# Optimization experiments

Measured on AMD Instinct MI355X. Metric: run time of the kernel, lower is better.

Reference implementation:

```python
import jax, jax.numpy as jnp
import numpy as np

N_NODES = 100000
N_EDGES = 1600000
HIDDEN = 64
N_LAYERS = 3
N_CLASSES = 2
N_GRAPHS = 128
NEG_SLOPE = 0.2  # PyG GATConv default negative_slope


def setup_inputs() -> dict:
    key = jax.random.key(0)
    ks = jax.random.split(key, 8)
    x = jax.random.randint(ks[0], (N_NODES,), 0, 2)
    edge_index = jax.random.randint(ks[1], (2, N_EDGES), 0, N_NODES)
    batch = jnp.sort(jax.random.randint(ks[2], (N_NODES,), 0, N_GRAPHS))
    scale = 1.0 / np.sqrt(HIDDEN)
    embed_table = jax.random.normal(ks[3], (2, HIDDEN), jnp.float32)
    Ws = jax.random.normal(ks[4], (N_LAYERS, HIDDEN, HIDDEN), jnp.float32) * scale
    a_srcs = jax.random.normal(ks[5], (N_LAYERS, HIDDEN), jnp.float32) * scale
    a_dsts = jax.random.normal(ks[6], (N_LAYERS, HIDDEN), jnp.float32) * scale
    biases = jnp.zeros((N_LAYERS, HIDDEN), jnp.float32)
    W_out = jax.random.normal(ks[7], (HIDDEN, N_CLASSES), jnp.float32) * scale
    b_out = jnp.zeros((N_CLASSES,), jnp.float32)
    return {"x": x, "edge_index": edge_index, "batch": batch,
            "embed_table": embed_table, "Ws": Ws, "a_srcs": a_srcs,
            "a_dsts": a_dsts, "biases": biases, "W_out": W_out, "b_out": b_out}


def _gat_layer(h, src, dst, W, a_s, a_d, b):
    # h: [N, D]; src/dst: [E'] (self loops included) -> PyG GATConv, heads=1
    hW = h @ W                                   # [N, D]
    e = jax.nn.leaky_relu((hW @ a_s)[src] + (hW @ a_d)[dst], NEG_SLOPE)  # [E']
    m = jax.ops.segment_max(e, dst, num_segments=N_NODES)               # stable softmax per dst
    ex = jnp.exp(e - m[dst])
    denom = jax.ops.segment_sum(ex, dst, num_segments=N_NODES)
    alpha = ex / denom[dst]                      # [E']
    out = jax.ops.segment_sum(hW[src] * alpha[:, None], dst, num_segments=N_NODES)
    return out + b


def reference(x, edge_index, batch, embed_table, Ws, a_srcs, a_dsts, biases, W_out, b_out):
    loop = jnp.arange(N_NODES)
    src = jnp.concatenate([edge_index[0], loop])  # PyG add_self_loops=True
    dst = jnp.concatenate([edge_index[1], loop])
    h = embed_table[x]                            # [N, D]
    for l in range(N_LAYERS):
        h = _gat_layer(h, src, dst, Ws[l], a_srcs[l], a_dsts[l], biases[l])
        if l < N_LAYERS - 1:
            h = jax.nn.relu(h)
    sums = jax.ops.segment_sum(h, batch, num_segments=N_GRAPHS)
    counts = jax.ops.segment_sum(jnp.ones((N_NODES,), h.dtype), batch, num_segments=N_GRAPHS)
    pooled = sums / jnp.maximum(counts, 1.0)[:, None]  # global_mean_pool
    return pooled @ W_out + b_out                      # [G, num_classes]
```

## Files before the change

### kernel.cpp

```cpp
#include <hip/hip_runtime.h>
#include <hip/hip_bf16.h>
#include <float.h>

#define N_NODES 100000
#define N_EDGES 1600000
#define HIDDEN 64
#define N_GRAPHS 128
#define NEG_SLOPE 0.2f
#define ETOT (N_EDGES + N_NODES)

#define BSHIFT 9
#define NB ((N_NODES + 511) >> BSHIFT)
#define PAIR_CHUNK 4096
#define PAIR_BLOCKS ((N_EDGES + PAIR_CHUNK - 1) / PAIR_CHUNK)
#define XBIT_BLOCKS ((N_NODES + 255) / 256)
#define TBL_BLOCKS (NLVL / 8)
#define CAP 12288

#define NREP 64
#define REP_STRIDE 272
#define NLVL 512

__device__ __forceinline__ unsigned short f2bf(float f) {
    unsigned u = __float_as_uint(f);
    unsigned r = (u + 0x7FFFu + ((u >> 16) & 1u)) >> 16;
    return (unsigned short)r;
}
__device__ __forceinline__ float blo(unsigned u) { return __uint_as_float(u << 16); }
__device__ __forceinline__ float bhi(unsigned u) { return __uint_as_float(u & 0xFFFF0000u); }
__device__ __forceinline__ int sb0(unsigned u) { return (int)((unsigned)(u << 24)) >> 24; }
__device__ __forceinline__ int sb1(unsigned u) { return (int)((unsigned)(u << 16)) >> 24; }
__device__ __forceinline__ int sb2(unsigned u) { return (int)((unsigned)(u << 8)) >> 24; }
__device__ __forceinline__ int sb3(unsigned u) { return (int)u >> 24; }


__global__ __launch_bounds__(256) void k_prep(
    const int* __restrict__ x,
    int* __restrict__ gcnt, float* __restrict__ pool_acc,
    unsigned* __restrict__ xb)
{
    int t = threadIdx.x, b = blockIdx.x;
    if (b == 0 && t < NB) gcnt[t] = 0;
    if (b < NREP && t < 2 * N_GRAPHS) pool_acc[b * REP_STRIDE + t] = 0.f;
    int i = b * 256 + t;
    int lane = t & 63;
    bool bb = (i < N_NODES) && (x[i] != 0);
    unsigned long long m = __ballot(bb);
    int wid = i >> 6;
    if (i < N_NODES + 64) {
        if (lane == 0) xb[wid * 2] = (unsigned)m;
        if (lane == 32) xb[wid * 2 + 1] = (unsigned)(m >> 32);
    }
}


__global__ __launch_bounds__(512) void k_scatter(
    const int* __restrict__ e0, const int* __restrict__ e1,
    const unsigned* __restrict__ xb, int* __restrict__ gcnt,
    int* __restrict__ pairs,
    const float* __restrict__ embed, const float* __restrict__ Ws,
    const float* __restrict__ biases, const float* __restrict__ a_srcs,
    const float* __restrict__ a_dsts, const float* __restrict__ W_out,
    unsigned char* __restrict__ Tq8, float* __restrict__ Tscl,
    float* __restrict__ Ts1s, float* __restrict__ Ts1d,
    float* __restrict__ sparams)
{
    __shared__ int hcnt[NB];
    __shared__ int base[NB];
    __shared__ int lstart[NB];
    __shared__ int tot[256];
    __shared__ int staged[PAIR_CHUNK];
    __shared__ int sdest[PAIR_CHUNK];
    int t = threadIdx.x, b = blockIdx.x;

    if (b >= PAIR_BLOCKS) {
        int l = (b - PAIR_BLOCKS) * 8 + (t >> 6);
        int f = t & 63;
        float r0 = 0.f, r1 = 0.f;
#pragma unroll 8
        for (int k = 0; k < 64; ++k) {
            float w = Ws[k * 64 + f];
            r0 = fmaf(embed[k], w, r0);
            r1 = fmaf(embed[64 + k], w, r1);
        }
        if (l == 0) {
            float as = a_srcs[f], ad = a_dsts[f];
            float t0 = r0 * as, t1 = r1 * as, t2 = r0 * ad, t3 = r1 * ad;
#pragma unroll
            for (int off = 32; off >= 1; off >>= 1) {
                t0 += __shfl_xor(t0, off); t1 += __shfl_xor(t1, off);
                t2 += __shfl_xor(t2, off); t3 += __shfl_xor(t3, off);
            }
            if (f == 0) { sparams[0] = t0; sparams[1] = t1; sparams[2] = t2; sparams[3] = t3; }
        }
        if (l == 1) {
            float b2 = biases[128 + f];
            float t4 = b2 * W_out[f * 2];
            float t5 = b2 * W_out[f * 2 + 1];
#pragma unroll
            for (int off = 32; off >= 1; off >>= 1) {
                t4 += __shfl_xor(t4, off); t5 += __shfl_xor(t5, off);
            }
            if (f == 0) { sparams[4] = t4; sparams[5] = t5; }
        }
        float c1 = (float)l * (1.f / (NLVL - 1));
        float o = fmaxf(biases[f] + r0 + c1 * (r1 - r0), 0.f);
        const float* W1 = Ws + 4096;
        float h = 0.f;
#pragma unroll 8
        for (int k = 0; k < 64; ++k) h = fmaf(__shfl(o, k), W1[k * 64 + f], h);
        float ss = h * a_srcs[64 + f];
        float sd = h * a_dsts[64 + f];
        float am = fabsf(h);
#pragma unroll
        for (int off = 32; off >= 1; off >>= 1) {
            ss += __shfl_xor(ss, off);
            sd += __shfl_xor(sd, off);
            am = fmaxf(am, __shfl_xor(am, off));
        }
        float iscl = (am > 0.f) ? 127.f / am : 0.f;
        Tq8[l * 64 + f] = (unsigned char)(__float2int_rn(h * iscl) & 255);
        if (f == 0) { Tscl[l] = am * (1.f / 127.f); Ts1s[l] = ss; Ts1d[l] = sd; }
        return;
    }

    if (t < NB) hcnt[t] = 0;
    __syncthreads();
    int ebase = b * PAIR_CHUNK;
    int ecount = min(PAIR_CHUNK, N_EDGES - ebase);
    for (int i = 4 * t; i < ecount; i += 2048) {
        int4 d4 = *(const int4*)(e1 + ebase + i);
        atomicAdd(&hcnt[d4.x >> BSHIFT], 1);
        atomicAdd(&hcnt[d4.y >> BSHIFT], 1);
        atomicAdd(&hcnt[d4.z >> BSHIFT], 1);
        atomicAdd(&hcnt[d4.w >> BSHIFT], 1);
    }
    __syncthreads();
    int v = (t < NB) ? hcnt[t] : 0;
    if (t < 256) tot[t] = v;
    __syncthreads();
    for (int off = 1; off < 256; off <<= 1) {
        int u = (t >= off && t < 256) ? tot[t - off] : 0;
        __syncthreads();
        if (t < 256) tot[t] += u;
        __syncthreads();
    }
    if (t < NB) {
        lstart[t] = tot[t] - v;
        base[t] = v ? atomicAdd(&gcnt[t], v) : 0;
        hcnt[t] = 0;
    }
    __syncthreads();
    for (int i = 4 * t; i < ecount; i += 2048) {
        int4 s4 = *(const int4*)(e0 + ebase + i);
        int4 d4 = *(const int4*)(e1 + ebase + i);
        int ss[4] = {s4.x, s4.y, s4.z, s4.w};
        int dd[4] = {d4.x, d4.y, d4.z, d4.w};
#pragma unroll
        for (int j = 0; j < 4; ++j) {
            int s = ss[j], d = dd[j];
            int xv = (xb[s >> 5] >> (s & 31)) & 1;
            int B = d >> BSHIFT;
            int idx = atomicAdd(&hcnt[B], 1);
            int lp = lstart[B] + idx;
            staged[lp] = (xv << 26) | ((d & 511) << 17) | s;
            sdest[lp] = B * CAP + base[B] + idx;
        }
    }
    __syncthreads();
    for (int i = t; i < ecount; i += 512)
        pairs[sdest[i]] = staged[i];
}

__global__ __launch_bounds__(1024) void k_csr_bucket(
    const int* __restrict__ pairs, const int* __restrict__ gcnt,
    const int* __restrict__ x, const float* __restrict__ sparams,
    int* __restrict__ rowptr, int* __restrict__ col,
    unsigned short* __restrict__ cidx)
{
    __shared__ int deg[512];
    __shared__ int excl[512];
    __shared__ int cnt2[512];
    __shared__ int wsum[16];
    __shared__ int p0sh;
    int b = blockIdx.x;
    int t = threadIdx.x;
    int nb = b << BSHIFT;
    int nodes = min(512, N_NODES - nb);

    int pv = (t < b) ? gcnt[t] : 0;
#pragma unroll
    for (int off = 32; off >= 1; off >>= 1) pv += __shfl_xor(pv, off);
    if ((t & 63) == 0) wsum[t >> 6] = pv;
    __syncthreads();
    if (t == 0) {
        int s = 0;
#pragma unroll
        for (int i = 0; i < 16; ++i) s += wsum[i];
        p0sh = s;
    }

    int xself = 0;
    if (t < 512) {
        xself = (t < nodes) ? (x[nb + t] & 1) : 0;
        deg[t] = (t < nodes) ? (1 | (xself << 16)) : 0;
        cnt2[t] = 1;
    }
    __syncthreads();
    int cnt = gcnt[b];
    int pbase = b * CAP;
    int cnt4 = cnt & ~3;
    for (int i = 4 * t; i < cnt4; i += 4096) {
        int4 p4 = *(const int4*)(pairs + pbase + i);
        atomicAdd(&deg[(p4.x >> 17) & 511], 1 | (((p4.x >> 26) & 1) << 16));
        atomicAdd(&deg[(p4.y >> 17) & 511], 1 | (((p4.y >> 26) & 1) << 16));
        atomicAdd(&deg[(p4.z >> 17) & 511], 1 | (((p4.z >> 26) & 1) << 16));
        atomicAdd(&deg[(p4.w >> 17) & 511], 1 | (((p4.w >> 26) & 1) << 16));
    }
    for (int i = cnt4 + t; i < cnt; i += 1024) {
        int p = pairs[pbase + i];
        atomicAdd(&deg[(p >> 17) & 511], 1 | (((p >> 26) & 1) << 16));
    }
    __syncthreads();

    int packed = (t < 512) ? deg[t] : 0;
    int val = packed & 0xFFFF;
    int kx = packed >> 16;
    if (t < nodes) {
        float ss0 = sparams[0], ss1 = sparams[1];
        float sd = xself ? sparams[3] : sparams[2];
        float e0 = ss0 + sd; e0 = (e0 >= 0.f) ? e0 : NEG_SLOPE * e0;
        float e1 = ss1 + sd; e1 = (e1 >= 0.f) ? e1 : NEG_SLOPE * e1;
        float pp0 = __expf(e0), pp1 = __expf(e1);
        float kn = (float)kx, dn = (float)(val - kx);
        float c1 = kn * pp1 / (dn * pp0 + kn * pp1);
        cidx[nb + t] = (unsigned short)__float2int_rn(c1 * (float)(NLVL - 1));
    }

    int xx = val;
#pragma unroll
    for (int off = 1; off < 64; off <<= 1) {
        int y = __shfl_up(xx, off);
        if ((t & 63) >= off) xx += y;
    }
    if ((t & 63) == 63 && t < 512) wsum[t >> 6] = xx;
    __syncthreads();
    if (t == 0) {
        int s = 0;
#pragma unroll
        for (int i = 0; i < 8; ++i) { int v = wsum[i]; wsum[i] = s; s += v; }
    }
    __syncthreads();
    int ex = xx - val + wsum[t >> 6];
    if (t < 512) excl[t] = ex;

    int p0 = p0sh;
    int colbase = p0 + nb;
    if (t < nodes) {
        rowptr[nb + t] = colbase + ex;
        col[colbase + ex] = nb + t;
    }
    if (b == NB - 1 && t == 0) rowptr[N_NODES] = ETOT;
    __syncthreads();
    for (int i = 4 * t; i < cnt4; i += 4096) {
        int4 p4 = *(const int4*)(pairs + pbase + i);
        int pp[4] = {p4.x, p4.y, p4.z, p4.w};
#pragma unroll
        for (int j = 0; j < 4; ++j) {
            int li = (pp[j] >> 17) & 511;
            int pos = colbase + excl[li] + atomicAdd(&cnt2[li], 1);
            col[pos] = pp[j] & 0x1FFFF;
        }
    }
    for (int i = cnt4 + t; i < cnt; i += 1024) {
        int p = pairs[pbase + i];
        int li = (p >> 17) & 511;
        int pos = colbase + excl[li] + atomicAdd(&cnt2[li], 1);
        col[pos] = p & 0x1FFFF;
    }
}


__global__ __launch_bounds__(256) void k_agg1(
    const unsigned char* __restrict__ Tq8, const float* __restrict__ Tscl,
    const float* __restrict__ Ts1s, const float* __restrict__ Ts1d,
    const unsigned short* __restrict__ cidx, const int* __restrict__ col,
    const int* __restrict__ rowptr, const float* __restrict__ bias,
    unsigned short* __restrict__ hout)
{
    __shared__ float2 stash[4][64];
    int t = threadIdx.x;
    int wave = t >> 6, lane = t & 63;
    int h = lane >> 5, hl = lane & 31;
    int base = blockIdx.x * 8 + wave * 2;
    if (base >= N_NODES) return;
    const char* hb = (const char*)Tq8;

    int node = base + h;
    bool valid = (node < N_NODES);
    int row = 0, end = 0;
    if (valid) { row = rowptr[node]; end = rowptr[node + 1]; }
    int deg = end - row;
    int degO = __shfl_xor(deg, 32);
    bool fast = (deg <= 32) && (degO <= 32);

    if (fast) {
        int idx = 0;
        float p = 0.f, sc = 0.f;
        if (hl < deg) idx = cidx[col[row + hl]];
        float sdi = Ts1d[__shfl(idx, h * 32)];
        if (hl < deg) {
            float ee = Ts1s[idx] + sdi;
            ee = (ee >= 0.f) ? ee : NEG_SLOPE * ee;
            p = __expf(ee);
            sc = Tscl[idx];
        }
        stash[wave][lane] = make_float2(p * sc, __int_as_float(idx * 64));

        int q = hl >> 4;
        int f = hl & 15;
        int f4 = f * 4;
        int sb = h * 32;
        float a0 = 0.f, a1 = 0.f, a2 = 0.f, a3 = 0.f;
        int degr = (deg + 7) & ~7;
        for (int j = q; j < degr; j += 8) {
            float2 e0 = stash[wave][sb + j];
            float2 e1 = stash[wave][sb + j + 2];
            float2 e2 = stash[wave][sb + j + 4];
            float2 e3 = stash[wave][sb + j + 6];
            unsigned v0 = *(const unsigned*)(hb + (__float_as_int(e0.y) + f4));
            unsigned v1 = *(const unsigned*)(hb + (__float_as_int(e1.y) + f4));
            unsigned v2 = *(const unsigned*)(hb + (__float_as_int(e2.y) + f4));
            unsigned v3 = *(const unsigned*)(hb + (__float_as_int(e3.y) + f4));
            a0 = fmaf(e0.x, (float)sb0(v0), a0);
            a1 = fmaf(e0.x, (float)sb1(v0), a1);
            a2 = fmaf(e0.x, (float)sb2(v0), a2);
            a3 = fmaf(e0.x, (float)sb3(v0), a3);
            a0 = fmaf(e1.x, (float)sb0(v1), a0);
            a1 = fmaf(e1.x, (float)sb1(v1), a1);
            a2 = fmaf(e1.x, (float)sb2(v1), a2);
            a3 = fmaf(e1.x, (float)sb3(v1), a3);
            a0 = fmaf(e2.x, (float)sb0(v2), a0);
            a1 = fmaf(e2.x, (float)sb1(v2), a1);
            a2 = fmaf(e2.x, (float)sb2(v2), a2);
            a3 = fmaf(e2.x, (float)sb3(v2), a3);
            a0 = fmaf(e3.x, (float)sb0(v3), a0);
            a1 = fmaf(e3.x, (float)sb1(v3), a1);
            a2 = fmaf(e3.x, (float)sb2(v3), a2);
            a3 = fmaf(e3.x, (float)sb3(v3), a3);
        }
        float denom = p;
#pragma unroll
        for (int off = 16; off >= 1; off >>= 1) denom += __shfl_xor(denom, off);
        float inv = 1.f / denom;
        a0 += __shfl_xor(a0, 16);
        a1 += __shfl_xor(a1, 16);
        a2 += __shfl_xor(a2, 16);
        a3 += __shfl_xor(a3, 16);
        if (hl < 16 && valid) {
            float4 bb = *(const float4*)&bias[4 * f];
            ushort4 pk;
            pk.x = f2bf(fmaxf(fmaf(a0, inv, bb.x), 0.f));
            pk.y = f2bf(fmaxf(fmaf(a1, inv, bb.y), 0.f));
            pk.z = f2bf(fmaxf(fmaf(a2, inv, bb.z), 0.f));
            pk.w = f2bf(fmaxf(fmaf(a3, inv, bb.w), 0.f));
            *(ushort4*)&hout[node * 64 + 4 * f] = pk;
        }
    } else {
        for (int s = 0; s < 2; ++s) {
            int nd = base + s;
            if (nd >= N_NODES) continue;
            int r = rowptr[nd], e = rowptr[nd + 1];
            float sdi = Ts1d[cidx[nd]];
            float m = -FLT_MAX;
            for (int j = r + lane; j < e; j += 64) {
                float ee = Ts1s[cidx[col[j]]] + sdi;
                ee = (ee >= 0.f) ? ee : NEG_SLOPE * ee;
                m = fmaxf(m, ee);
            }
#pragma unroll
            for (int off = 32; off >= 1; off >>= 1) m = fmaxf(m, __shfl_xor(m, off));
            float denom = 0.f;
            for (int j = r + lane; j < e; j += 64) {
                float ee = Ts1s[cidx[col[j]]] + sdi;
                ee = (ee >= 0.f) ? ee : NEG_SLOPE * ee;
                denom += __expf(ee - m);
            }
#pragma unroll
            for (int off = 32; off >= 1; off >>= 1) denom += __shfl_xor(denom, off);
            float inv = 1.f / denom;
            float acc = 0.f;
            for (int j = r; j < e; ++j) {
                int idxj = cidx[col[j]];
                float ee = Ts1s[idxj] + sdi;
                ee = (ee >= 0.f) ? ee : NEG_SLOPE * ee;
                float w = __expf(ee - m) * inv * Tscl[idxj];
                int bq = (int)(signed char)Tq8[idxj * 64 + lane];
                acc = fmaf(w, (float)bq, acc);
            }
            hout[nd * 64 + lane] = f2bf(fmaxf(acc + bias[lane], 0.f));
        }
    }
}


__global__ __launch_bounds__(256) void k_gemm2(
    const unsigned* __restrict__ h32, const float* __restrict__ W,
    const float* __restrict__ a_s, const float* __restrict__ a_d,
    const float* __restrict__ W_out,
    float4* __restrict__ szz)
{
    __shared__ float Wl[64 * 64];
    __shared__ float hT[64 * 68];
    int t = threadIdx.x;
    int r0 = blockIdx.x * 64;

    for (int i = t; i < 4096; i += 256) Wl[i] = W[i];
    for (int i = t; i < 2048; i += 256) {
        int r = i >> 5, m = i & 31;
        int row = r0 + r;
        unsigned u = (row < N_NODES) ? h32[row * 32 + m] : 0u;
        hT[(2 * m) * 68 + r]     = blo(u);
        hT[(2 * m + 1) * 68 + r] = bhi(u);
    }
    __syncthreads();

    int tcol = t & 15;
    int trow = t >> 4;
    float acc[4][4];
#pragma unroll
    for (int i = 0; i < 4; ++i)
#pragma unroll
        for (int j = 0; j < 4; ++j) acc[i][j] = 0.f;

    for (int k = 0; k < 64; ++k) {
        float4 va = *(const float4*)&hT[k * 68 + trow * 4];
        float4 vb = *(const float4*)&Wl[k * 64 + tcol * 4];
        float a[4] = {va.x, va.y, va.z, va.w};
        float bb[4] = {vb.x, vb.y, vb.z, vb.w};
#pragma unroll
        for (int i = 0; i < 4; ++i)
#pragma unroll
            for (int j = 0; j < 4; ++j) acc[i][j] = fmaf(a[i], bb[j], acc[i][j]);
    }

    float4 as4 = *(const float4*)&a_s[tcol * 4];
    float4 ad4 = *(const float4*)&a_d[tcol * 4];
    float asr[4] = {as4.x, as4.y, as4.z, as4.w};
    float adr[4] = {ad4.x, ad4.y, ad4.z, ad4.w};
    float4 wa = *(const float4*)&W_out[8 * tcol];
    float4 wb = *(const float4*)&W_out[8 * tcol + 4];

#pragma unroll
    for (int i = 0; i < 4; ++i) {
        int row = r0 + trow * 4 + i;
        float ps = 0.f, pd = 0.f;
#pragma unroll
        for (int j = 0; j < 4; ++j) {
            ps = fmaf(acc[i][j], asr[j], ps);
            pd = fmaf(acc[i][j], adr[j], pd);
        }
        float z0 = acc[i][0] * wa.x + acc[i][1] * wa.z + acc[i][2] * wb.x + acc[i][3] * wb.z;
        float z1 = acc[i][0] * wa.y + acc[i][1] * wa.w + acc[i][2] * wb.y + acc[i][3] * wb.w;
#pragma unroll
        for (int off = 8; off >= 1; off >>= 1) {
            ps += __shfl_xor(ps, off);
            pd += __shfl_xor(pd, off);
            z0 += __shfl_xor(z0, off);
            z1 += __shfl_xor(z1, off);
        }
        if (row < N_NODES && tcol == 0) {
            szz[row] = make_float4(ps, z0, z1, pd);
        }
    }
}


__global__ __launch_bounds__(256) void k_pool2(
    const float4* __restrict__ szz, const int* __restrict__ col,
    const int* __restrict__ rowptr, const int* __restrict__ batch,
    float* __restrict__ pool_acc)
{
    __shared__ int rp2[33];
    int t = threadIdx.x;
    int wave = t >> 6, lane = t & 63;
    int h = lane >> 5, hl = lane & 31;
    int nb0 = blockIdx.x * 32;
    if (t < 33) {
        int n = nb0 + t;
        rp2[t] = (n <= N_NODES) ? rowptr[n] : ETOT;
    }
    __syncthreads();
    float* rep = pool_acc + ((blockIdx.x * 4 + wave) & (NREP - 1)) * REP_STRIDE;

    int gcur = -1;
    float acc0 = 0.f, acc1 = 0.f;

#pragma unroll
    for (int i = 0; i < 4; ++i) {
        int nls = wave * 8 + 2 * i + h;
        int node = nb0 + nls;
        bool valid = (node < N_NODES);
        int row = valid ? rp2[nls] : 0;
        int end = valid ? rp2[nls + 1] : 0;
        int deg = end - row;
        int degO = __shfl_xor(deg, 32);
        bool fast = (deg <= 32) && (degO <= 32);
        float r0 = 0.f, r1 = 0.f;

        if (fast) {
            float sdi = valid ? szz[node].w : 0.f;
            float p = 0.f, zy = 0.f, zz = 0.f;
            if (hl < deg) {
                int c = col[row + hl];
                float4 sz = szz[c];
                float ee = sz.x + sdi;
                ee = (ee >= 0.f) ? ee : NEG_SLOPE * ee;
                p = __expf(ee);
                zy = sz.y; zz = sz.z;
            }
            float n0 = p * zy, n1 = p * zz, dn = p;
#pragma unroll
            for (int off = 16; off >= 1; off >>= 1) {
                n0 += __shfl_xor(n0, off);
                n1 += __shfl_xor(n1, off);
                dn += __shfl_xor(dn, off);
            }
            float inv = 1.f / dn;
            r0 = n0 * inv; r1 = n1 * inv;
        } else {
            float rr0[2], rr1[2];
#pragma unroll
            for (int s = 0; s < 2; ++s) {
                rr0[s] = rr1[s] = 0.f;
                int nds = wave * 8 + 2 * i + s;
                int nd = nb0 + nds;
                if (nd >= N_NODES) continue;
                int r = rp2[nds], e = rp2[nds + 1];
                float sdi = szz[nd].w;
                float n0 = 0.f, n1 = 0.f, dn = 0.f;
                for (int j = r + lane; j < e; j += 64) {
                    int c = col[j];
                    float4 sz = szz[c];
                    float ee = sz.x + sdi;
                    ee = (ee >= 0.f) ? ee : NEG_SLOPE * ee;
                    float p = __expf(ee);
                    n0 = fmaf(p, sz.y, n0);
                    n1 = fmaf(p, sz.z, n1);
                    dn += p;
                }
#pragma unroll
                for (int off = 32; off >= 1; off >>= 1) {
                    n0 += __shfl_xor(n0, off);
                    n1 += __shfl_xor(n1, off);
                    dn += __shfl_xor(dn, off);
                }
                float inv = 1.f / dn;
                rr0[s] = n0 * inv; rr1[s] = n1 * inv;
            }
            r0 = rr0[h]; r1 = rr1[h];
        }

        if (hl == 0 && valid) {
            int g = batch[node];
            if (g != gcur) {
                if (gcur >= 0) {
                    atomicAdd(&rep[gcur * 2], acc0);
                    atomicAdd(&rep[gcur * 2 + 1], acc1);
                }
                gcur = g; acc0 = r0; acc1 = r1;
            } else {
                acc0 += r0; acc1 += r1;
            }
        }
    }
    if (hl == 0 && gcur >= 0) {
        atomicAdd(&rep[gcur * 2], acc0);
        atomicAdd(&rep[gcur * 2 + 1], acc1);
    }
}


__device__ __forceinline__ int lower_bound_dev(const int* __restrict__ a, int n, int v) {
    int lo = 0, hi = n;
    while (lo < hi) {
        int mid = (lo + hi) >> 1;
        if (a[mid] < v) lo = mid + 1; else hi = mid;
    }
    return lo;
}

__global__ void k_head(const float* __restrict__ pool_acc,
                       const int* __restrict__ batch,
                       const float* __restrict__ b_out,
                       const float* __restrict__ sparams,
                       float* __restrict__ out)
{
    int t = threadIdx.x;
    if (t < 2 * N_GRAPHS) {
        float s = 0.f;
#pragma unroll 8
        for (int r = 0; r < NREP; ++r) s += pool_acc[r * REP_STRIDE + t];
        int g = t >> 1, c = t & 1;
        int start = lower_bound_dev(batch, N_NODES, g);
        int end = lower_bound_dev(batch, N_NODES, g + 1);
        float cnt = fmaxf((float)(end - start), 1.f);
        out[t] = s / cnt + sparams[4 + c] + b_out[c];
    }
}


extern "C" void kernel_launch(void* const* d_in, const int* in_sizes, int n_in,
                              void* d_out, int out_size, void* d_ws, size_t ws_size,
                              hipStream_t stream) {
    const int*   x       = (const int*)d_in[0];
    const int*   edge    = (const int*)d_in[1];
    const int*   batch   = (const int*)d_in[2];
    const float* embed   = (const float*)d_in[3];
    const float* Ws      = (const float*)d_in[4];
    const float* a_srcs  = (const float*)d_in[5];
    const float* a_dsts  = (const float*)d_in[6];
    const float* biases  = (const float*)d_in[7];
    const float* W_out   = (const float*)d_in[8];
    const float* b_out   = (const float*)d_in[9];
    float* out = (float*)d_out;

    char* ws = (char*)d_ws;
    size_t off = 0;
    auto alloc = [&](size_t bytes) -> void* {
        void* p = ws + off;
        off += (bytes + 255) & ~(size_t)255;
        return p;
    };
    unsigned short* hout  = (unsigned short*)alloc((size_t)N_NODES * 64 * sizeof(unsigned short));
    float4* szz     = (float4*)alloc((size_t)N_NODES * sizeof(float4));
    unsigned short* cidx = (unsigned short*)alloc((size_t)N_NODES * sizeof(unsigned short));
    int*   rowptr   = (int*)alloc((size_t)(N_NODES + 1) * sizeof(int));
    int*   colA     = (int*)alloc((size_t)ETOT * sizeof(int));
    int*   gcnt     = (int*)alloc((size_t)NB * sizeof(int));
    float* pool_acc = (float*)alloc((size_t)(NREP * REP_STRIDE) * sizeof(float));
    unsigned* xb    = (unsigned*)alloc((size_t)3232 * sizeof(unsigned));
    unsigned char* Tq8 = (unsigned char*)alloc((size_t)NLVL * 64);
    float* Tscl     = (float*)alloc((size_t)NLVL * sizeof(float));
    float* Ts1s     = (float*)alloc((size_t)NLVL * sizeof(float));
    float* Ts1d     = (float*)alloc((size_t)NLVL * sizeof(float));
    float* sparams  = (float*)alloc((size_t)8 * sizeof(float));
    int*   pairs    = (int*)alloc((size_t)NB * CAP * sizeof(int));

    const int* e0 = edge;
    const int* e1 = edge + N_EDGES;

    k_prep<<<XBIT_BLOCKS, 256, 0, stream>>>(x, gcnt, pool_acc, xb);
    k_scatter<<<PAIR_BLOCKS + TBL_BLOCKS, 512, 0, stream>>>(
        e0, e1, xb, gcnt, pairs,
        embed, Ws, biases, a_srcs, a_dsts, W_out,
        Tq8, Tscl, Ts1s, Ts1d, sparams);
    k_csr_bucket<<<NB, 1024, 0, stream>>>(pairs, gcnt, x, sparams, rowptr, colA, cidx);

    k_agg1<<<(N_NODES + 7) / 8, 256, 0, stream>>>(
        Tq8, Tscl, Ts1s, Ts1d, cidx, colA, rowptr, biases + 64, hout);
    k_gemm2<<<(N_NODES + 63) / 64, 256, 0, stream>>>(
        (const unsigned*)hout, Ws + 8192, a_srcs + 128, a_dsts + 128, W_out, szz);
    k_pool2<<<(N_NODES + 31) / 32, 256, 0, stream>>>(
        szz, colA, rowptr, batch, pool_acc);
    k_head<<<1, 256, 0, stream>>>(pool_acc, batch, b_out, sparams, out);
}
```

Before: 198.4 us.

## Fold layer-3 weight projections into layer-2 aggregation, removing the GEMM kernel

Precomputes a 64x4 matrix Vp = W3 · [a_src, W_out0, W_out1, a_dst] in an extra block of the scatter kernel. The layer-2 aggregation then projects each node's hidden vector directly onto these four columns and writes the float4 szz. This drops the separate k_gemm2 launch and the bf16 hidden-state round trip through global memory. It relies on linearity (h·W3)·v = h·(W3·v) and adds a few shuffles to the aggregation kernel. It also removes the bf16 rounding of the intermediate.

```diff
diff --git a/kernel.cpp b/kernel.cpp
--- a/kernel.cpp
+++ b/kernel.cpp
@@ -21,13 +21,6 @@
 #define REP_STRIDE 272
 #define NLVL 512
 
-__device__ __forceinline__ unsigned short f2bf(float f) {
-    unsigned u = __float_as_uint(f);
-    unsigned r = (u + 0x7FFFu + ((u >> 16) & 1u)) >> 16;
-    return (unsigned short)r;
-}
-__device__ __forceinline__ float blo(unsigned u) { return __uint_as_float(u << 16); }
-__device__ __forceinline__ float bhi(unsigned u) { return __uint_as_float(u & 0xFFFF0000u); }
 __device__ __forceinline__ int sb0(unsigned u) { return (int)((unsigned)(u << 24)) >> 24; }
 __device__ __forceinline__ int sb1(unsigned u) { return (int)((unsigned)(u << 16)) >> 24; }
 __device__ __forceinline__ int sb2(unsigned u) { return (int)((unsigned)(u << 8)) >> 24; }
@@ -63,7 +56,7 @@
     const float* __restrict__ a_dsts, const float* __restrict__ W_out,
     unsigned char* __restrict__ Tq8, float* __restrict__ Tscl,
     float* __restrict__ Ts1s, float* __restrict__ Ts1d,
-    float* __restrict__ sparams)
+    float* __restrict__ sparams, float* __restrict__ Vp)
 {
     __shared__ int hcnt[NB];
     __shared__ int base[NB];
@@ -72,6 +65,24 @@
     __shared__ int staged[PAIR_CHUNK];
     __shared__ int sdest[PAIR_CHUNK];
     int t = threadIdx.x, b = blockIdx.x;
+
+    if (b >= PAIR_BLOCKS + TBL_BLOCKS) {
+        int w = t >> 6, f = t & 63;
+        if (w < 4) {
+            const float* W3 = Ws + 8192;
+            float s = 0.f;
+#pragma unroll 8
+            for (int m = 0; m < 64; ++m) {
+                float u = (w == 0) ? a_srcs[128 + m]
+                        : (w == 1) ? W_out[2 * m]
+                        : (w == 2) ? W_out[2 * m + 1]
+                        : a_dsts[128 + m];
+                s = fmaf(W3[f * 64 + m], u, s);
+            }
+            Vp[f * 4 + w] = s;
+        }
+        return;
+    }
 
     if (b >= PAIR_BLOCKS) {
         int l = (b - PAIR_BLOCKS) * 8 + (t >> 6);
@@ -286,7 +297,7 @@
     const float* __restrict__ Ts1s, const float* __restrict__ Ts1d,
     const unsigned short* __restrict__ cidx, const int* __restrict__ col,
     const int* __restrict__ rowptr, const float* __restrict__ bias,
-    unsigned short* __restrict__ hout)
+    const float4* __restrict__ Vp, float4* __restrict__ szz)
 {
     __shared__ float2 stash[4][64];
     int t = threadIdx.x;
@@ -357,15 +368,31 @@
         a1 += __shfl_xor(a1, 16);
         a2 += __shfl_xor(a2, 16);
         a3 += __shfl_xor(a3, 16);
+
+        float4 pr = make_float4(0.f, 0.f, 0.f, 0.f);
         if (hl < 16 && valid) {
             float4 bb = *(const float4*)&bias[4 * f];
-            ushort4 pk;
-            pk.x = f2bf(fmaxf(fmaf(a0, inv, bb.x), 0.f));
-            pk.y = f2bf(fmaxf(fmaf(a1, inv, bb.y), 0.f));
-            pk.z = f2bf(fmaxf(fmaf(a2, inv, bb.z), 0.f));
-            pk.w = f2bf(fmaxf(fmaf(a3, inv, bb.w), 0.f));
-            *(ushort4*)&hout[node * 64 + 4 * f] = pk;
-        }
+            float h0 = fmaxf(fmaf(a0, inv, bb.x), 0.f);
+            float h1 = fmaxf(fmaf(a1, inv, bb.y), 0.f);
+            float h2 = fmaxf(fmaf(a2, inv, bb.z), 0.f);
+            float h3 = fmaxf(fmaf(a3, inv, bb.w), 0.f);
+            float4 w0 = Vp[4 * f + 0];
+            float4 w1 = Vp[4 * f + 1];
+            float4 w2 = Vp[4 * f + 2];
+            float4 w3 = Vp[4 * f + 3];
+            pr.x = h0 * w0.x + h1 * w1.x + h2 * w2.x + h3 * w3.x;
+            pr.y = h0 * w0.y + h1 * w1.y + h2 * w2.y + h3 * w3.y;
+            pr.z = h0 * w0.z + h1 * w1.z + h2 * w2.z + h3 * w3.z;
+            pr.w = h0 * w0.w + h1 * w1.w + h2 * w2.w + h3 * w3.w;
+        }
+#pragma unroll
+        for (int off = 8; off >= 1; off >>= 1) {
+            pr.x += __shfl_xor(pr.x, off);
+            pr.y += __shfl_xor(pr.y, off);
+            pr.z += __shfl_xor(pr.z, off);
+            pr.w += __shfl_xor(pr.w, off);
+        }
+        if (hl == 0 && valid) szz[node] = pr;
     } else {
         for (int s = 0; s < 2; ++s) {
             int nd = base + s;
@@ -398,79 +425,17 @@
                 int bq = (int)(signed char)Tq8[idxj * 64 + lane];
                 acc = fmaf(w, (float)bq, acc);
             }
-            hout[nd * 64 + lane] = f2bf(fmaxf(acc + bias[lane], 0.f));
-        }
-    }
-}
-
-
-__global__ __launch_bounds__(256) void k_gemm2(
-    const unsigned* __restrict__ h32, const float* __restrict__ W,
-    const float* __restrict__ a_s, const float* __restrict__ a_d,
-    const float* __restrict__ W_out,
-    float4* __restrict__ szz)
-{
-    __shared__ float Wl[64 * 64];
-    __shared__ float hT[64 * 68];
-    int t = threadIdx.x;
-    int r0 = blockIdx.x * 64;
-
-    for (int i = t; i < 4096; i += 256) Wl[i] = W[i];
-    for (int i = t; i < 2048; i += 256) {
-        int r = i >> 5, m = i & 31;
-        int row = r0 + r;
-        unsigned u = (row < N_NODES) ? h32[row * 32 + m] : 0u;
-        hT[(2 * m) * 68 + r]     = blo(u);
-        hT[(2 * m + 1) * 68 + r] = bhi(u);
-    }
-    __syncthreads();
-
-    int tcol = t & 15;
-    int trow = t >> 4;
-    float acc[4][4];
-#pragma unroll
-    for (int i = 0; i < 4; ++i)
-#pragma unroll
-        for (int j = 0; j < 4; ++j) acc[i][j] = 0.f;
-
-    for (int k = 0; k < 64; ++k) {
-        float4 va = *(const float4*)&hT[k * 68 + trow * 4];
-        float4 vb = *(const float4*)&Wl[k * 64 + tcol * 4];
-        float a[4] = {va.x, va.y, va.z, va.w};
-        float bb[4] = {vb.x, vb.y, vb.z, vb.w};
-#pragma unroll
-        for (int i = 0; i < 4; ++i)
-#pragma unroll
-            for (int j = 0; j < 4; ++j) acc[i][j] = fmaf(a[i], bb[j], acc[i][j]);
-    }
-
-    float4 as4 = *(const float4*)&a_s[tcol * 4];
-    float4 ad4 = *(const float4*)&a_d[tcol * 4];
-    float asr[4] = {as4.x, as4.y, as4.z, as4.w};
-    float adr[4] = {ad4.x, ad4.y, ad4.z, ad4.w};
-    float4 wa = *(const float4*)&W_out[8 * tcol];
-    float4 wb = *(const float4*)&W_out[8 * tcol + 4];
-
-#pragma unroll
-    for (int i = 0; i < 4; ++i) {
-        int row = r0 + trow * 4 + i;
-        float ps = 0.f, pd = 0.f;
-#pragma unroll
-        for (int j = 0; j < 4; ++j) {
-            ps = fmaf(acc[i][j], asr[j], ps);
-            pd = fmaf(acc[i][j], adr[j], pd);
-        }
-        float z0 = acc[i][0] * wa.x + acc[i][1] * wa.z + acc[i][2] * wb.x + acc[i][3] * wb.z;
-        float z1 = acc[i][0] * wa.y + acc[i][1] * wa.w + acc[i][2] * wb.y + acc[i][3] * wb.w;
-#pragma unroll
-        for (int off = 8; off >= 1; off >>= 1) {
-            ps += __shfl_xor(ps, off);
-            pd += __shfl_xor(pd, off);
-            z0 += __shfl_xor(z0, off);
-            z1 += __shfl_xor(z1, off);
-        }
-        if (row < N_NODES && tcol == 0) {
-            szz[row] = make_float4(ps, z0, z1, pd);
+            float hv = fmaxf(acc + bias[lane], 0.f);
+            float4 vp = Vp[lane];
+            float4 pr = make_float4(hv * vp.x, hv * vp.y, hv * vp.z, hv * vp.w);
+#pragma unroll
+            for (int off = 32; off >= 1; off >>= 1) {
+                pr.x += __shfl_xor(pr.x, off);
+                pr.y += __shfl_xor(pr.y, off);
+                pr.z += __shfl_xor(pr.z, off);
+                pr.w += __shfl_xor(pr.w, off);
+            }
+            if (lane == 0) szz[nd] = pr;
         }
     }
 }
@@ -632,7 +597,6 @@
         off += (bytes + 255) & ~(size_t)255;
         return p;
     };
-    unsigned short* hout  = (unsigned short*)alloc((size_t)N_NODES * 64 * sizeof(unsigned short));
     float4* szz     = (float4*)alloc((size_t)N_NODES * sizeof(float4));
     unsigned short* cidx = (unsigned short*)alloc((size_t)N_NODES * sizeof(unsigned short));
     int*   rowptr   = (int*)alloc((size_t)(N_NODES + 1) * sizeof(int));
@@ -645,22 +609,22 @@
     float* Ts1s     = (float*)alloc((size_t)NLVL * sizeof(float));
     float* Ts1d     = (float*)alloc((size_t)NLVL * sizeof(float));
     float* sparams  = (float*)alloc((size_t)8 * sizeof(float));
+    float* Vp       = (float*)alloc((size_t)256 * sizeof(float));
     int*   pairs    = (int*)alloc((size_t)NB * CAP * sizeof(int));
 
     const int* e0 = edge;
     const int* e1 = edge + N_EDGES;
 
     k_prep<<<XBIT_BLOCKS, 256, 0, stream>>>(x, gcnt, pool_acc, xb);
-    k_scatter<<<PAIR_BLOCKS + TBL_BLOCKS, 512, 0, stream>>>(
+    k_scatter<<<PAIR_BLOCKS + TBL_BLOCKS + 1, 512, 0, stream>>>(
         e0, e1, xb, gcnt, pairs,
         embed, Ws, biases, a_srcs, a_dsts, W_out,
-        Tq8, Tscl, Ts1s, Ts1d, sparams);
+        Tq8, Tscl, Ts1s, Ts1d, sparams, Vp);
     k_csr_bucket<<<NB, 1024, 0, stream>>>(pairs, gcnt, x, sparams, rowptr, colA, cidx);
 
     k_agg1<<<(N_NODES + 7) / 8, 256, 0, stream>>>(
-        Tq8, Tscl, Ts1s, Ts1d, cidx, colA, rowptr, biases + 64, hout);
-    k_gemm2<<<(N_NODES + 63) / 64, 256, 0, stream>>>(
-        (const unsigned*)hout, Ws + 8192, a_srcs + 128, a_dsts + 128, W_out, szz);
+        Tq8, Tscl, Ts1s, Ts1d, cidx, colA, rowptr, biases + 64,
+        (const float4*)Vp, szz);
     k_pool2<<<(N_NODES + 31) / 32, 256, 0, stream>>>(
         szz, colA, rowptr, batch, pool_acc);
     k_head<<<1, 256, 0, stream>>>(pool_acc, batch, b_out, sparams, out);
```

Result: faster. 181.9 us (-8.3%).
